# Kernel tuning notes

Hardware: AMD Instinct MI355X
Metric: run time of the kernel (lower is better)

The kernel has to match this reference:

```python
import jax, jax.numpy as jnp
import numpy as np
import math

GROUPS = 32  # min(256 // 4, 32)
EPS = 1e-5

def group_norm(x, w, b):
    B, C, H, W = x.shape
    xg = x.reshape(B, GROUPS, C // GROUPS, H, W)
    mean = jnp.mean(xg, axis=(2, 3, 4), keepdims=True)
    var = jnp.var(xg, axis=(2, 3, 4), keepdims=True)
    xn = ((xg - mean) * jax.lax.rsqrt(var + EPS)).reshape(B, C, H, W)
    return xn * w[None, :, None, None] + b[None, :, None, None]

def nin(x, W, b):
    # 1x1 projection: [B,C,H,W] x [C,D] -> [B,D,H,W]
    return jnp.einsum('bchw,cd->bdhw', x, W) + b[None, :, None, None]

def setup_inputs() -> dict:
    key = jax.random.key(0)
    ks = jax.random.split(key, 5)
    C = 256
    scale = 1.0 / math.sqrt(C)
    return {
        'x': jax.random.normal(ks[0], (4, C, 64, 64), dtype=jnp.float32),
        'gn_w': jnp.ones((C,), jnp.float32),
        'gn_b': jnp.zeros((C,), jnp.float32),
        'Wq': jax.random.normal(ks[1], (C, C), jnp.float32) * scale,
        'bq': jnp.zeros((C,), jnp.float32),
        'Wk': jax.random.normal(ks[2], (C, C), jnp.float32) * scale,
        'bk': jnp.zeros((C,), jnp.float32),
        'Wv': jax.random.normal(ks[3], (C, C), jnp.float32) * scale,
        'bv': jnp.zeros((C,), jnp.float32),
        'Wp': jax.random.normal(ks[4], (C, C), jnp.float32) * scale,
        'bp': jnp.zeros((C,), jnp.float32),
    }

def reference(x, gn_w, gn_b, Wq, bq, Wk, bk, Wv, bv, Wp, bp):
    B, C, H, W = x.shape
    h = group_norm(x, gn_w, gn_b)
    q = nin(h, Wq, bq).reshape(B, C, H * W)
    k = nin(h, Wk, bk).reshape(B, C, H * W)
    v = nin(h, Wv, bv).reshape(B, C, H * W)
    # attention logits: [B, HW, HW]
    w = jnp.einsum('bcn,bcm->bnm', q, k) * (C ** -0.5)
    w = jax.nn.softmax(w, axis=-1)
    h_out = jnp.einsum('bnm,bcm->bcn', w, v).reshape(B, C, H, W)
    h_out = nin(h_out, Wp, bp)
    out = x + h_out
    return out / math.sqrt(2.0)  # skip_rescale=True
```

## Files before the change

kernel.cpp:

```cpp
#include <hip/hip_runtime.h>
#include <math.h>


#define BB 4
#define CCH 256
#define NSP 4096
#define EPSV 1e-5f
#define ATTN_SCALE 0.0625f
#define RSQRT2 0.70710678118654752440f
#define KSPLIT 2
#define TILES_PER_PART 32

typedef __attribute__((ext_vector_type(8))) short bf16x8;
typedef __attribute__((ext_vector_type(4))) float f32x4;

typedef __attribute__((address_space(1))) void gvoid;
typedef __attribute__((address_space(3))) void lvoid;
__device__ __forceinline__ void dma16(const void* g, void* l) {
  __builtin_amdgcn_global_load_lds((gvoid*)g, (lvoid*)l, 16, 0, 0);
}

__device__ __forceinline__ short f2bf(float f) {
  union { float f; unsigned u; } a; a.f = f;
  unsigned r = a.u + 0x7fffu + ((a.u >> 16) & 1u);
  return (short)(r >> 16);
}
__device__ __forceinline__ float bf2f(short s) {
  union { unsigned u; float f; } a;
  a.u = ((unsigned)(unsigned short)s) << 16;
  return a.f;
}
__device__ __forceinline__ unsigned cvt_pk_bf16(float lo, float hi) {
  unsigned r;
  asm("v_cvt_pk_bf16_f32 %0, %1, %2" : "=v"(r) : "v"(lo), "v"(hi));
  return r;
}

__global__ __launch_bounds__(256) void gn_stats(
    const float* __restrict__ x, float* __restrict__ stats) {
  int b = blockIdx.x >> 5;
  int g = blockIdx.x & 31;
  size_t base = ((size_t)b * CCH + (size_t)g * 8) * NSP;
  const float4* xv = (const float4*)(x + base);
  int tid = threadIdx.x;
  float s = 0.f, ss = 0.f;
  for (int i = tid; i < 8192; i += 256) {
    float4 v = xv[i];
    s += (v.x + v.y) + (v.z + v.w);
    ss += (v.x * v.x + v.y * v.y) + (v.z * v.z + v.w * v.w);
  }
#pragma unroll
  for (int off = 32; off > 0; off >>= 1) {
    s += __shfl_down(s, off, 64);
    ss += __shfl_down(ss, off, 64);
  }
  __shared__ float rs[4], rss[4];
  int wv = tid >> 6;
  if ((tid & 63) == 0) { rs[wv] = s; rss[wv] = ss; }
  __syncthreads();
  if (tid == 0) {
    float S = rs[0] + rs[1] + rs[2] + rs[3];
    float SS = rss[0] + rss[1] + rss[2] + rss[3];
    float mean = S * (1.f / 32768.f);
    float var = SS * (1.f / 32768.f) - mean * mean;
    stats[(b * 32 + g) * 2 + 0] = mean;
    stats[(b * 32 + g) * 2 + 1] = rsqrtf(var + EPSV);
  }
}

__global__ __launch_bounds__(256) void prep_w(
    const float* __restrict__ Wq, const float* __restrict__ Wk,
    const float* __restrict__ Wv, const float* __restrict__ Wp,
    short* __restrict__ wts) {
  __shared__ float T[64][65];
  int c0 = blockIdx.x * 64, d0 = blockIdx.y * 64;
  int wz = blockIdx.z;
  const float* W = (wz == 0) ? Wq : (wz == 1) ? Wk : (wz == 2) ? Wv : Wp;
  short* wt = wts + (size_t)wz * CCH * CCH;
  int tid = threadIdx.x;
#pragma unroll
  for (int i = 0; i < 16; ++i) {
    int idx = tid + 256 * i;
    int row = idx >> 6, col = idx & 63;
    T[row][col] = W[(size_t)(c0 + row) * CCH + d0 + col];
  }
  __syncthreads();
#pragma unroll
  for (int i = 0; i < 16; ++i) {
    int idx = tid + 256 * i;
    int dr = idx >> 6, cc = idx & 63;
    wt[(size_t)(d0 + dr) * CCH + c0 + cc] = f2bf(T[cc][dr]);
  }
}

__global__ __launch_bounds__(512) void qkvg_kernel(
    const float* __restrict__ x, const float* __restrict__ stats,
    const float* __restrict__ gw, const float* __restrict__ gb,
    const short* __restrict__ wqt, const short* __restrict__ wkt,
    const short* __restrict__ wvt,
    const float* __restrict__ bq, const float* __restrict__ bk,
    const float* __restrict__ bv,
    short* __restrict__ qo, short* __restrict__ ko, short* __restrict__ vo) {
  __shared__ __align__(16) unsigned char smem[52224];
  float (*Ts)[68] = (float(*)[68])smem;
  float* aco = (float*)(smem + 17408);
  float* bco = aco + 256;
  short* Hs = (short*)(smem + 19456);
  short* Fo = (short*)smem;

  int bx = blockIdx.x;
  int b = bx & 3, n0 = (bx >> 2) * 64;
  int tid = threadIdx.x;
  if (tid < 256) {
    int g = tid >> 3;
    float mean = stats[(b * 32 + g) * 2 + 0];
    float rstd = stats[(b * 32 + g) * 2 + 1];
    float a = gw[tid] * rstd;
    aco[tid] = a;
    bco[tid] = gb[tid] - mean * a;
  }
  __syncthreads();
  const float* xb = x + (size_t)b * CCH * NSP;
  for (int p = 0; p < 4; ++p) {
    int c0 = p * 64;
#pragma unroll
    for (int i = 0; i < 2; ++i) {
      int crow = (tid >> 4) + i * 32;
      int c = c0 + crow;
      float4 v = *(const float4*)&xb[(size_t)c * NSP + n0 + (tid & 15) * 4];
      float a = aco[c], bb = bco[c];
      v.x = v.x * a + bb; v.y = v.y * a + bb;
      v.z = v.z * a + bb; v.w = v.w * a + bb;
      *(float4*)&Ts[crow][(tid & 15) * 4] = v;
    }
    __syncthreads();
    {
      int n = tid >> 3, seg = tid & 7;
      int cb = seg * 8;
      bf16x8 r;
#pragma unroll
      for (int j = 0; j < 8; ++j) r[j] = f2bf(Ts[cb + j][n]);
      int chunk = (c0 + cb) >> 3;
      *(bf16x8*)(Hs + n * 256 + ((chunk ^ (n & 7)) * 8)) = r;
    }
    __syncthreads();
  }
  int w = tid >> 6, lane = tid & 63, quad = lane >> 4, l16 = lane & 15;
  int wr = w & 3, h = w >> 2;
  bf16x8 a_h[8];
  {
    int row = wr * 16 + l16;
#pragma unroll
    for (int kc = 0; kc < 8; ++kc)
      a_h[kc] = *(bf16x8*)(Hs + row * 256 + (((kc * 4 + quad) ^ (row & 7)) * 8));
  }
  __syncthreads();
  for (int op = 0; op < 3; ++op) {
    const short* wt = (op == 0) ? wqt : (op == 1) ? wkt : wvt;
    const float* bias = (op == 0) ? bq : (op == 1) ? bk : bv;
    f32x4 acc[8];
#pragma unroll
    for (int mb = 0; mb < 8; ++mb) acc[mb] = (f32x4){0.f, 0.f, 0.f, 0.f};
#pragma unroll 4
    for (int mb = 0; mb < 8; ++mb) {
      const short* wp = wt + (size_t)((h * 8 + mb) * 16 + l16) * CCH + quad * 8;
#pragma unroll
      for (int kc = 0; kc < 8; ++kc) {
        bf16x8 af = *(const bf16x8*)(wp + kc * 32);
        acc[mb] = __builtin_amdgcn_mfma_f32_16x16x32_bf16(af, a_h[kc], acc[mb], 0, 0, 0);
      }
    }
    int n = n0 + wr * 16 + l16;
    if (op == 2) {
      short* ob = vo + (size_t)b * CCH * NSP;
      int mm = n & 63, m0_ = n & ~63;
      int mb_ = mm >> 4, qq = (mm >> 2) & 3, rr2 = mm & 3;
      int lc = (mb_ & 1) * 4 + qq;
      int jj = (mb_ >> 1) * 4 + rr2;
      int basen = m0_ + jj;
#pragma unroll
      for (int mb = 0; mb < 8; ++mb)
#pragma unroll
        for (int r = 0; r < 4; ++r) {
          int d = (h * 8 + mb) * 16 + quad * 4 + r;
          ob[(size_t)d * NSP + basen + ((lc ^ (d & 7)) << 3)] =
              f2bf(acc[mb][r] + bias[d]);
        }
    } else {
      float sc = (op == 0) ? ATTN_SCALE : 1.f;
      int nl = wr * 16 + l16;
#pragma unroll
      for (int mb = 0; mb < 8; ++mb)
#pragma unroll
        for (int r = 0; r < 4; ++r) {
          int d = (h * 8 + mb) * 16 + quad * 4 + r;
          Fo[nl * 264 + d] = f2bf((acc[mb][r] + bias[d]) * sc);
        }
      __syncthreads();
      short* ob = ((op == 0) ? qo : ko) + (size_t)b * NSP * CCH;
      {
        int row = tid >> 3, seg = tid & 7, r7 = row & 7;
        short* dst = ob + (size_t)(n0 + row) * CCH + seg * 32;
#pragma unroll
        for (int i = 0; i < 4; ++i) {
          int xch = seg * 4 + i;
          int cs = (xch & 24) | ((xch & 7) ^ r7);
          *(bf16x8*)(dst + i * 8) = *(bf16x8*)(Fo + row * 264 + cs * 8);
        }
      }
      __syncthreads();
    }
  }
}

__global__ __launch_bounds__(512, 1) void attn_kernel(
    const short* __restrict__ q, const short* __restrict__ k,
    const short* __restrict__ v, short* __restrict__ po,
    float* __restrict__ pm, float* __restrict__ pl) {
  __shared__ __align__(16) unsigned char smem[131072];
  short* Ks0 = (short*)smem;
  short* Ks1 = (short*)(smem + 32768);
  short* Vs0 = (short*)(smem + 65536);
  short* Vs1 = (short*)(smem + 98304);
  short* Fo  = (short*)smem;

  int bx = blockIdx.x;
  int grp = bx & 7;
  int b = grp & 3;
  int kh = grp >> 2;
  int n0 = ((bx >> 3) & 31) << 7;
  const short* qb = q + (size_t)b * NSP * CCH;
  const short* kb = k + (size_t)b * NSP * CCH;
  const char*  vbB = (const char*)(v + (size_t)b * CCH * NSP);
  int tid = threadIdx.x;
  int w = tid >> 6, lane = tid & 63, quad = lane >> 4, l16 = lane & 15;
  int mbase = kh * TILES_PER_PART * 64;

  bf16x8 a_q[8];
#pragma unroll
  for (int p = 0; p < 2; ++p) {
#pragma unroll
    for (int i = 0; i < 4; ++i) {
      int off = tid * 16 + i * 8192;
      dma16((const char*)(qb + (size_t)(n0 + p * 64) * CCH) + off,
            (char*)Ks0 + off);
    }
    __syncthreads();
    if ((w >> 2) == p) {
      int row = (w & 3) * 16 + l16;
#pragma unroll
      for (int kc = 0; kc < 8; ++kc)
        a_q[kc] = *(bf16x8*)(Ks0 + row * 256 + (((kc * 4 + quad) ^ (row & 7)) * 8));
    }
    __syncthreads();
  }

#pragma unroll
  for (int i = 0; i < 4; ++i) {
    int off = tid * 16 + i * 8192;
    dma16((const char*)(kb + (size_t)mbase * CCH) + off, (char*)Ks0 + off);
    int c = off >> 7, inrow = off & 127;
    dma16(vbB + (size_t)c * (NSP * 2) + (size_t)mbase * 2 + inrow,
          (char*)Vs0 + off);
  }
  __syncthreads();
#pragma unroll
  for (int i = 0; i < 4; ++i) {
    int off = tid * 16 + i * 8192;
    dma16((const char*)(kb + (size_t)(mbase + 64) * CCH) + off,
          (char*)Ks1 + off);
  }
  f32x4 s_prev[4];
#pragma unroll
  for (int mb = 0; mb < 4; ++mb) s_prev[mb] = (f32x4){0.f, 0.f, 0.f, 0.f};
  __builtin_amdgcn_s_setprio(1);
#pragma unroll
  for (int kc = 0; kc < 8; ++kc) {
#pragma unroll
    for (int mb = 0; mb < 4; ++mb) {
      int row = mb * 16 + l16;
      bf16x8 kf = *(bf16x8*)(Ks0 + row * 256 + (((kc * 4 + quad) ^ (row & 7)) * 8));
      s_prev[mb] = __builtin_amdgcn_mfma_f32_16x16x32_bf16(kf, a_q[kc], s_prev[mb], 0, 0, 0);
    }
  }
  __builtin_amdgcn_s_setprio(0);
  float mx_c = -1e30f;
#pragma unroll
  for (int mb = 0; mb < 4; ++mb)
#pragma unroll
    for (int r = 0; r < 4; ++r) mx_c = fmaxf(mx_c, s_prev[mb][r]);
  mx_c = fmaxf(mx_c, __shfl_xor(mx_c, 16));
  mx_c = fmaxf(mx_c, __shfl_xor(mx_c, 32));

  f32x4 accO[16];
#pragma unroll
  for (int cb = 0; cb < 16; ++cb) accO[cb] = (f32x4){0.f, 0.f, 0.f, 0.f};
  float m_run = -1e30f, l_run = 0.f;
  int pc0 = quad ^ (l16 & 7);
  int pc1 = (4 + quad) ^ (l16 & 7);

#pragma unroll 1
  for (int t = 0; t < TILES_PER_PART; ++t) {
    __syncthreads();
    short* Kd = (t & 1) ? Ks1 : Ks0;
    short* Kr = (t & 1) ? Ks0 : Ks1;
    short* Vd = (t & 1) ? Vs0 : Vs1;
    short* Vr = (t & 1) ? Vs1 : Vs0;
    if (t + 2 < TILES_PER_PART) {
      const char* kp = (const char*)(kb + (size_t)(mbase + (t + 2) * 64) * CCH);
#pragma unroll
      for (int i = 0; i < 4; ++i) {
        int off = tid * 16 + i * 8192;
        dma16(kp + off, (char*)Kd + off);
      }
    }
    if (t + 1 < TILES_PER_PART) {
      int m0 = mbase + (t + 1) * 64;
#pragma unroll
      for (int i = 0; i < 4; ++i) {
        int off = tid * 16 + i * 8192;
        int c = off >> 7, inrow = off & 127;
        dma16(vbB + (size_t)c * (NSP * 2) + (size_t)m0 * 2 + inrow,
              (char*)Vd + off);
      }
    }
    f32x4 sn[4];
#pragma unroll
    for (int mb = 0; mb < 4; ++mb) sn[mb] = (f32x4){0.f, 0.f, 0.f, 0.f};
    if (t + 1 < TILES_PER_PART) {
      __builtin_amdgcn_s_setprio(1);
#pragma unroll
      for (int kc = 0; kc < 8; ++kc) {
#pragma unroll
        for (int mb = 0; mb < 4; ++mb) {
          int row = mb * 16 + l16;
          bf16x8 kf = *(bf16x8*)(Kr + row * 256 + (((kc * 4 + quad) ^ (row & 7)) * 8));
          sn[mb] = __builtin_amdgcn_mfma_f32_16x16x32_bf16(kf, a_q[kc], sn[mb], 0, 0, 0);
        }
      }
      __builtin_amdgcn_s_setprio(0);
    }
    if (!__all(mx_c - m_run <= 8.f)) {
      float mnew = fmaxf(m_run, mx_c);
      float alpha = __expf(m_run - mnew);
#pragma unroll
      for (int cb = 0; cb < 16; ++cb) accO[cb] *= alpha;
      l_run *= alpha;
      m_run = mnew;
    }
    float ls = 0.f;
#pragma unroll
    for (int mb = 0; mb < 4; ++mb)
#pragma unroll
      for (int r = 0; r < 4; ++r) {
        float p = __expf(s_prev[mb][r] - m_run);
        ls += p;
        s_prev[mb][r] = p;
      }
    ls += __shfl_xor(ls, 16);
    ls += __shfl_xor(ls, 32);
    l_run += ls;
    union { unsigned u[4]; bf16x8 v; } pw0, pw1;
    pw0.u[0] = cvt_pk_bf16(s_prev[0][0], s_prev[0][1]);
    pw0.u[1] = cvt_pk_bf16(s_prev[0][2], s_prev[0][3]);
    pw0.u[2] = cvt_pk_bf16(s_prev[2][0], s_prev[2][1]);
    pw0.u[3] = cvt_pk_bf16(s_prev[2][2], s_prev[2][3]);
    pw1.u[0] = cvt_pk_bf16(s_prev[1][0], s_prev[1][1]);
    pw1.u[1] = cvt_pk_bf16(s_prev[1][2], s_prev[1][3]);
    pw1.u[2] = cvt_pk_bf16(s_prev[3][0], s_prev[3][1]);
    pw1.u[3] = cvt_pk_bf16(s_prev[3][2], s_prev[3][3]);
    __builtin_amdgcn_s_setprio(1);
#pragma unroll
    for (int cb = 0; cb < 16; ++cb) {
      bf16x8 vf = *(bf16x8*)(Vr + (cb * 16 + l16) * 64 + pc0 * 8);
      accO[cb] = __builtin_amdgcn_mfma_f32_16x16x32_bf16(vf, pw0.v, accO[cb], 0, 0, 0);
    }
#pragma unroll
    for (int cb = 0; cb < 16; ++cb) {
      bf16x8 vf = *(bf16x8*)(Vr + (cb * 16 + l16) * 64 + pc1 * 8);
      accO[cb] = __builtin_amdgcn_mfma_f32_16x16x32_bf16(vf, pw1.v, accO[cb], 0, 0, 0);
    }
    __builtin_amdgcn_s_setprio(0);
    if (t + 1 < TILES_PER_PART) {
      float mxn = -1e30f;
#pragma unroll
      for (int mb = 0; mb < 4; ++mb)
#pragma unroll
        for (int r = 0; r < 4; ++r) mxn = fmaxf(mxn, sn[mb][r]);
      mxn = fmaxf(mxn, __shfl_xor(mxn, 16));
      mxn = fmaxf(mxn, __shfl_xor(mxn, 32));
      mx_c = mxn;
    }
#pragma unroll
    for (int mb = 0; mb < 4; ++mb) s_prev[mb] = sn[mb];
  }
  size_t sbase = ((size_t)kh * BB + b) * NSP + n0;
  if (quad == 0) {
    pm[sbase + w * 16 + l16] = m_run;
    pl[sbase + w * 16 + l16] = l_run;
  }
  float linv = 1.f / l_run;
  short* ob = po + ((size_t)kh * BB + b) * NSP * CCH;
#pragma unroll
  for (int p = 0; p < 2; ++p) {
    __syncthreads();
    if ((w >> 2) == p) {
      int nloc = (w & 3) * 16 + l16;
#pragma unroll
      for (int cb = 0; cb < 16; ++cb)
#pragma unroll
        for (int r = 0; r < 4; ++r)
          Fo[nloc * 264 + cb * 16 + quad * 4 + r] = f2bf(accO[cb][r] * linv);
    }
    __syncthreads();
    int row = tid >> 3, seg = tid & 7;
    short* dst = ob + (size_t)(n0 + p * 64 + row) * CCH + seg * 32;
#pragma unroll
    for (int i = 0; i < 4; ++i)
      *(bf16x8*)(dst + i * 8) = *(bf16x8*)(Fo + row * 264 + seg * 32 + i * 8);
  }
}

__global__ __launch_bounds__(256) void proj_kernel(
    const short* __restrict__ po, const float* __restrict__ pm,
    const float* __restrict__ pl, const short* __restrict__ wpt,
    const float* __restrict__ bp, const float* __restrict__ x,
    float* __restrict__ out) {
  int n0 = blockIdx.x * 64;
  int dh = blockIdx.y * 128;
  int b = blockIdx.z;
  int tid = threadIdx.x;
  int w = tid >> 6, lane = tid & 63, quad = lane >> 4, l16 = lane & 15;
  int n = n0 + w * 16 + l16;

  float wgt[KSPLIT];
  {
    float m[KSPLIT];
    float M = -1e30f;
#pragma unroll
    for (int s = 0; s < KSPLIT; ++s) {
      m[s] = pm[((size_t)s * BB + b) * NSP + n];
      M = fmaxf(M, m[s]);
    }
    float wsum = 0.f;
#pragma unroll
    for (int s = 0; s < KSPLIT; ++s) {
      wgt[s] = __expf(m[s] - M) * pl[((size_t)s * BB + b) * NSP + n];
      wsum += wgt[s];
    }
    float linv = 1.f / wsum;
#pragma unroll
    for (int s = 0; s < KSPLIT; ++s) wgt[s] *= linv;
  }

  f32x4 acc[8];
#pragma unroll
  for (int mb = 0; mb < 8; ++mb) acc[mb] = (f32x4){0.f, 0.f, 0.f, 0.f};

  const short* pob = po + ((size_t)b * NSP + n) * CCH;
#pragma unroll 2
  for (int kc = 0; kc < 8; ++kc) {
    int coff = kc * 32 + quad * 8;
    float e[8];
#pragma unroll
    for (int i = 0; i < 8; ++i) e[i] = 0.f;
#pragma unroll
    for (int s = 0; s < KSPLIT; ++s) {
      bf16x8 f = *(const bf16x8*)(pob + (size_t)s * BB * NSP * CCH + coff);
#pragma unroll
      for (int i = 0; i < 8; ++i) e[i] += wgt[s] * bf2f(f[i]);
    }
    bf16x8 bm;
#pragma unroll
    for (int i = 0; i < 8; ++i) bm[i] = f2bf(e[i]);
#pragma unroll
    for (int mb = 0; mb < 8; ++mb) {
      bf16x8 af = *(const bf16x8*)(wpt + (size_t)(dh + mb * 16 + l16) * CCH + coff);
      acc[mb] = __builtin_amdgcn_mfma_f32_16x16x32_bf16(af, bm, acc[mb], 0, 0, 0);
    }
  }
#pragma unroll
  for (int mb = 0; mb < 8; ++mb) {
#pragma unroll
    for (int r = 0; r < 4; ++r) {
      int d = dh + mb * 16 + quad * 4 + r;
      size_t off = ((size_t)b * CCH + d) * NSP + n;
      out[off] = (acc[mb][r] + bp[d] + x[off]) * RSQRT2;
    }
  }
}

extern "C" void kernel_launch(void* const* d_in, const int* in_sizes, int n_in,
                              void* d_out, int out_size, void* d_ws, size_t ws_size,
                              hipStream_t stream) {
  const float* x  = (const float*)d_in[0];
  const float* gw = (const float*)d_in[1];
  const float* gb = (const float*)d_in[2];
  const float* Wq = (const float*)d_in[3];
  const float* bq = (const float*)d_in[4];
  const float* Wk = (const float*)d_in[5];
  const float* bk = (const float*)d_in[6];
  const float* Wv = (const float*)d_in[7];
  const float* bv = (const float*)d_in[8];
  const float* Wp = (const float*)d_in[9];
  const float* bp = (const float*)d_in[10];
  float* out = (float*)d_out;

  const size_t SZ = (size_t)BB * CCH * NSP;
  short* qb  = (short*)d_ws;
  short* kb  = qb + SZ;
  short* vb  = kb + SZ;
  short* poT = vb + SZ;
  float* pm  = (float*)(poT + (size_t)KSPLIT * SZ);
  float* pl  = pm + (size_t)KSPLIT * BB * NSP;
  float* stats = pl + (size_t)KSPLIT * BB * NSP;
  short* wts = (short*)(stats + BB * 64);
  short* wqt = wts;
  short* wkt = wts + (size_t)CCH * CCH;
  short* wvt = wts + (size_t)2 * CCH * CCH;
  short* wpt = wts + (size_t)3 * CCH * CCH;

  gn_stats<<<dim3(BB * 32), dim3(256), 0, stream>>>(x, stats);
  prep_w<<<dim3(4, 4, 4), dim3(256), 0, stream>>>(Wq, Wk, Wv, Wp, wts);
  qkvg_kernel<<<dim3(256), dim3(512), 0, stream>>>(
      x, stats, gw, gb, wqt, wkt, wvt, bq, bk, bv, qb, kb, vb);
  attn_kernel<<<dim3(BB * 32 * KSPLIT), dim3(512), 0, stream>>>(
      qb, kb, vb, poT, pm, pl);
  proj_kernel<<<dim3(64, 2, BB), dim3(256), 0, stream>>>(
      poT, pm, pl, wpt, bp, x, out);
}
```

Measured before the change: 275.4 us.

## Halve attention block to 4 waves, each wave handling 32 query rows

The attention kernel now launches 256 threads instead of 512, and each wave computes two 16-row query subtiles. Every K and V fragment read from LDS feeds two MFMAs, which halves LDS read traffic per unit of compute. The DMA loops and the output writeback are adjusted to the smaller thread count. The cost is roughly double the accumulator and score registers per wave, with fewer waves per CU available to hide latency.

```diff
diff --git a/kernel.cpp b/kernel.cpp
--- a/kernel.cpp
+++ b/kernel.cpp
@@ -213,7 +213,7 @@
   }
 }
 
-__global__ __launch_bounds__(512, 1) void attn_kernel(
+__global__ __launch_bounds__(256, 1) void attn_kernel(
     const short* __restrict__ q, const short* __restrict__ k,
     const short* __restrict__ v, short* __restrict__ po,
     float* __restrict__ pm, float* __restrict__ pl) {
@@ -236,28 +236,32 @@
   int w = tid >> 6, lane = tid & 63, quad = lane >> 4, l16 = lane & 15;
   int mbase = kh * TILES_PER_PART * 64;
 
-  bf16x8 a_q[8];
+  bf16x8 a_q[2][8];
 #pragma unroll
   for (int p = 0; p < 2; ++p) {
 #pragma unroll
-    for (int i = 0; i < 4; ++i) {
-      int off = tid * 16 + i * 8192;
+    for (int i = 0; i < 8; ++i) {
+      int off = tid * 16 + i * 4096;
       dma16((const char*)(qb + (size_t)(n0 + p * 64) * CCH) + off,
             (char*)Ks0 + off);
     }
     __syncthreads();
-    if ((w >> 2) == p) {
-      int row = (w & 3) * 16 + l16;
-#pragma unroll
-      for (int kc = 0; kc < 8; ++kc)
-        a_q[kc] = *(bf16x8*)(Ks0 + row * 256 + (((kc * 4 + quad) ^ (row & 7)) * 8));
-    }
-    __syncthreads();
-  }
-
-#pragma unroll
-  for (int i = 0; i < 4; ++i) {
-    int off = tid * 16 + i * 8192;
+    if ((w >> 1) == p) {
+#pragma unroll
+      for (int qh = 0; qh < 2; ++qh) {
+        int row = (w & 1) * 32 + qh * 16 + l16;
+#pragma unroll
+        for (int kc = 0; kc < 8; ++kc)
+          a_q[qh][kc] =
+              *(bf16x8*)(Ks0 + row * 256 + (((kc * 4 + quad) ^ (row & 7)) * 8));
+      }
+    }
+    __syncthreads();
+  }
+
+#pragma unroll
+  for (int i = 0; i < 8; ++i) {
+    int off = tid * 16 + i * 4096;
     dma16((const char*)(kb + (size_t)mbase * CCH) + off, (char*)Ks0 + off);
     int c = off >> 7, inrow = off & 127;
     dma16(vbB + (size_t)c * (NSP * 2) + (size_t)mbase * 2 + inrow,
@@ -265,14 +269,16 @@
   }
   __syncthreads();
 #pragma unroll
-  for (int i = 0; i < 4; ++i) {
-    int off = tid * 16 + i * 8192;
+  for (int i = 0; i < 8; ++i) {
+    int off = tid * 16 + i * 4096;
     dma16((const char*)(kb + (size_t)(mbase + 64) * CCH) + off,
           (char*)Ks1 + off);
   }
-  f32x4 s_prev[4];
-#pragma unroll
-  for (int mb = 0; mb < 4; ++mb) s_prev[mb] = (f32x4){0.f, 0.f, 0.f, 0.f};
+  f32x4 s_prev[4][2];
+#pragma unroll
+  for (int mb = 0; mb < 4; ++mb)
+#pragma unroll
+    for (int qh = 0; qh < 2; ++qh) s_prev[mb][qh] = (f32x4){0.f, 0.f, 0.f, 0.f};
   __builtin_amdgcn_s_setprio(1);
 #pragma unroll
   for (int kc = 0; kc < 8; ++kc) {
@@ -280,22 +286,32 @@
     for (int mb = 0; mb < 4; ++mb) {
       int row = mb * 16 + l16;
       bf16x8 kf = *(bf16x8*)(Ks0 + row * 256 + (((kc * 4 + quad) ^ (row & 7)) * 8));
-      s_prev[mb] = __builtin_amdgcn_mfma_f32_16x16x32_bf16(kf, a_q[kc], s_prev[mb], 0, 0, 0);
+#pragma unroll
+      for (int qh = 0; qh < 2; ++qh)
+        s_prev[mb][qh] = __builtin_amdgcn_mfma_f32_16x16x32_bf16(
+            kf, a_q[qh][kc], s_prev[mb][qh], 0, 0, 0);
     }
   }
   __builtin_amdgcn_s_setprio(0);
-  float mx_c = -1e30f;
-#pragma unroll
-  for (int mb = 0; mb < 4; ++mb)
-#pragma unroll
-    for (int r = 0; r < 4; ++r) mx_c = fmaxf(mx_c, s_prev[mb][r]);
-  mx_c = fmaxf(mx_c, __shfl_xor(mx_c, 16));
-  mx_c = fmaxf(mx_c, __shfl_xor(mx_c, 32));
-
-  f32x4 accO[16];
-#pragma unroll
-  for (int cb = 0; cb < 16; ++cb) accO[cb] = (f32x4){0.f, 0.f, 0.f, 0.f};
-  float m_run = -1e30f, l_run = 0.f;
+  float mx_c[2];
+#pragma unroll
+  for (int qh = 0; qh < 2; ++qh) {
+    float mx = -1e30f;
+#pragma unroll
+    for (int mb = 0; mb < 4; ++mb)
+#pragma unroll
+      for (int r = 0; r < 4; ++r) mx = fmaxf(mx, s_prev[mb][qh][r]);
+    mx = fmaxf(mx, __shfl_xor(mx, 16));
+    mx = fmaxf(mx, __shfl_xor(mx, 32));
+    mx_c[qh] = mx;
+  }
+
+  f32x4 accO[16][2];
+#pragma unroll
+  for (int cb = 0; cb < 16; ++cb)
+#pragma unroll
+    for (int qh = 0; qh < 2; ++qh) accO[cb][qh] = (f32x4){0.f, 0.f, 0.f, 0.f};
+  float m_run[2] = {-1e30f, -1e30f}, l_run[2] = {0.f, 0.f};
   int pc0 = quad ^ (l16 & 7);
   int pc1 = (4 + quad) ^ (l16 & 7);
 
@@ -309,24 +325,26 @@
     if (t + 2 < TILES_PER_PART) {
       const char* kp = (const char*)(kb + (size_t)(mbase + (t + 2) * 64) * CCH);
 #pragma unroll
-      for (int i = 0; i < 4; ++i) {
-        int off = tid * 16 + i * 8192;
+      for (int i = 0; i < 8; ++i) {
+        int off = tid * 16 + i * 4096;
         dma16(kp + off, (char*)Kd + off);
       }
     }
     if (t + 1 < TILES_PER_PART) {
       int m0 = mbase + (t + 1) * 64;
 #pragma unroll
-      for (int i = 0; i < 4; ++i) {
-        int off = tid * 16 + i * 8192;
+      for (int i = 0; i < 8; ++i) {
+        int off = tid * 16 + i * 4096;
         int c = off >> 7, inrow = off & 127;
         dma16(vbB + (size_t)c * (NSP * 2) + (size_t)m0 * 2 + inrow,
               (char*)Vd + off);
       }
     }
-    f32x4 sn[4];
-#pragma unroll
-    for (int mb = 0; mb < 4; ++mb) sn[mb] = (f32x4){0.f, 0.f, 0.f, 0.f};
+    f32x4 sn[4][2];
+#pragma unroll
+    for (int mb = 0; mb < 4; ++mb)
+#pragma unroll
+      for (int qh = 0; qh < 2; ++qh) sn[mb][qh] = (f32x4){0.f, 0.f, 0.f, 0.f};
     if (t + 1 < TILES_PER_PART) {
       __builtin_amdgcn_s_setprio(1);
 #pragma unroll
@@ -335,89 +353,120 @@
         for (int mb = 0; mb < 4; ++mb) {
           int row = mb * 16 + l16;
           bf16x8 kf = *(bf16x8*)(Kr + row * 256 + (((kc * 4 + quad) ^ (row & 7)) * 8));
-          sn[mb] = __builtin_amdgcn_mfma_f32_16x16x32_bf16(kf, a_q[kc], sn[mb], 0, 0, 0);
+#pragma unroll
+          for (int qh = 0; qh < 2; ++qh)
+            sn[mb][qh] = __builtin_amdgcn_mfma_f32_16x16x32_bf16(
+                kf, a_q[qh][kc], sn[mb][qh], 0, 0, 0);
         }
       }
       __builtin_amdgcn_s_setprio(0);
     }
-    if (!__all(mx_c - m_run <= 8.f)) {
-      float mnew = fmaxf(m_run, mx_c);
-      float alpha = __expf(m_run - mnew);
-#pragma unroll
-      for (int cb = 0; cb < 16; ++cb) accO[cb] *= alpha;
-      l_run *= alpha;
-      m_run = mnew;
-    }
-    float ls = 0.f;
-#pragma unroll
-    for (int mb = 0; mb < 4; ++mb)
-#pragma unroll
-      for (int r = 0; r < 4; ++r) {
-        float p = __expf(s_prev[mb][r] - m_run);
-        ls += p;
-        s_prev[mb][r] = p;
-      }
-    ls += __shfl_xor(ls, 16);
-    ls += __shfl_xor(ls, 32);
-    l_run += ls;
-    union { unsigned u[4]; bf16x8 v; } pw0, pw1;
-    pw0.u[0] = cvt_pk_bf16(s_prev[0][0], s_prev[0][1]);
-    pw0.u[1] = cvt_pk_bf16(s_prev[0][2], s_prev[0][3]);
-    pw0.u[2] = cvt_pk_bf16(s_prev[2][0], s_prev[2][1]);
-    pw0.u[3] = cvt_pk_bf16(s_prev[2][2], s_prev[2][3]);
-    pw1.u[0] = cvt_pk_bf16(s_prev[1][0], s_prev[1][1]);
-    pw1.u[1] = cvt_pk_bf16(s_prev[1][2], s_prev[1][3]);
-    pw1.u[2] = cvt_pk_bf16(s_prev[3][0], s_prev[3][1]);
-    pw1.u[3] = cvt_pk_bf16(s_prev[3][2], s_prev[3][3]);
+    bool grow = (mx_c[0] - m_run[0] > 8.f) || (mx_c[1] - m_run[1] > 8.f);
+    if (__any(grow)) {
+#pragma unroll
+      for (int qh = 0; qh < 2; ++qh) {
+        float mnew = fmaxf(m_run[qh], mx_c[qh]);
+        float alpha = __expf(m_run[qh] - mnew);
+#pragma unroll
+        for (int cb = 0; cb < 16; ++cb) accO[cb][qh] *= alpha;
+        l_run[qh] *= alpha;
+        m_run[qh] = mnew;
+      }
+    }
+#pragma unroll
+    for (int qh = 0; qh < 2; ++qh) {
+      float ls = 0.f;
+#pragma unroll
+      for (int mb = 0; mb < 4; ++mb)
+#pragma unroll
+        for (int r = 0; r < 4; ++r) {
+          float p = __expf(s_prev[mb][qh][r] - m_run[qh]);
+          ls += p;
+          s_prev[mb][qh][r] = p;
+        }
+      ls += __shfl_xor(ls, 16);
+      ls += __shfl_xor(ls, 32);
+      l_run[qh] += ls;
+    }
+    union { unsigned u[4]; bf16x8 v; } pw0[2], pw1[2];
+#pragma unroll
+    for (int qh = 0; qh < 2; ++qh) {
+      pw0[qh].u[0] = cvt_pk_bf16(s_prev[0][qh][0], s_prev[0][qh][1]);
+      pw0[qh].u[1] = cvt_pk_bf16(s_prev[0][qh][2], s_prev[0][qh][3]);
+      pw0[qh].u[2] = cvt_pk_bf16(s_prev[2][qh][0], s_prev[2][qh][1]);
+      pw0[qh].u[3] = cvt_pk_bf16(s_prev[2][qh][2], s_prev[2][qh][3]);
+      pw1[qh].u[0] = cvt_pk_bf16(s_prev[1][qh][0], s_prev[1][qh][1]);
+      pw1[qh].u[1] = cvt_pk_bf16(s_prev[1][qh][2], s_prev[1][qh][3]);
+      pw1[qh].u[2] = cvt_pk_bf16(s_prev[3][qh][0], s_prev[3][qh][1]);
+      pw1[qh].u[3] = cvt_pk_bf16(s_prev[3][qh][2], s_prev[3][qh][3]);
+    }
     __builtin_amdgcn_s_setprio(1);
 #pragma unroll
     for (int cb = 0; cb < 16; ++cb) {
       bf16x8 vf = *(bf16x8*)(Vr + (cb * 16 + l16) * 64 + pc0 * 8);
-      accO[cb] = __builtin_amdgcn_mfma_f32_16x16x32_bf16(vf, pw0.v, accO[cb], 0, 0, 0);
+#pragma unroll
+      for (int qh = 0; qh < 2; ++qh)
+        accO[cb][qh] = __builtin_amdgcn_mfma_f32_16x16x32_bf16(
+            vf, pw0[qh].v, accO[cb][qh], 0, 0, 0);
     }
 #pragma unroll
     for (int cb = 0; cb < 16; ++cb) {
       bf16x8 vf = *(bf16x8*)(Vr + (cb * 16 + l16) * 64 + pc1 * 8);
-      accO[cb] = __builtin_amdgcn_mfma_f32_16x16x32_bf16(vf, pw1.v, accO[cb], 0, 0, 0);
+#pragma unroll
+      for (int qh = 0; qh < 2; ++qh)
+        accO[cb][qh] = __builtin_amdgcn_mfma_f32_16x16x32_bf16(
+            vf, pw1[qh].v, accO[cb][qh], 0, 0, 0);
     }
     __builtin_amdgcn_s_setprio(0);
     if (t + 1 < TILES_PER_PART) {
-      float mxn = -1e30f;
-#pragma unroll
-      for (int mb = 0; mb < 4; ++mb)
-#pragma unroll
-        for (int r = 0; r < 4; ++r) mxn = fmaxf(mxn, sn[mb][r]);
-      mxn = fmaxf(mxn, __shfl_xor(mxn, 16));
-      mxn = fmaxf(mxn, __shfl_xor(mxn, 32));
-      mx_c = mxn;
-    }
-#pragma unroll
-    for (int mb = 0; mb < 4; ++mb) s_prev[mb] = sn[mb];
+#pragma unroll
+      for (int qh = 0; qh < 2; ++qh) {
+        float mxn = -1e30f;
+#pragma unroll
+        for (int mb = 0; mb < 4; ++mb)
+#pragma unroll
+          for (int r = 0; r < 4; ++r) mxn = fmaxf(mxn, sn[mb][qh][r]);
+        mxn = fmaxf(mxn, __shfl_xor(mxn, 16));
+        mxn = fmaxf(mxn, __shfl_xor(mxn, 32));
+        mx_c[qh] = mxn;
+      }
+    }
+#pragma unroll
+    for (int mb = 0; mb < 4; ++mb)
+#pragma unroll
+      for (int qh = 0; qh < 2; ++qh) s_prev[mb][qh] = sn[mb][qh];
   }
   size_t sbase = ((size_t)kh * BB + b) * NSP + n0;
   if (quad == 0) {
-    pm[sbase + w * 16 + l16] = m_run;
-    pl[sbase + w * 16 + l16] = l_run;
-  }
-  float linv = 1.f / l_run;
+#pragma unroll
+    for (int qh = 0; qh < 2; ++qh) {
+      pm[sbase + w * 32 + qh * 16 + l16] = m_run[qh];
+      pl[sbase + w * 32 + qh * 16 + l16] = l_run[qh];
+    }
+  }
   short* ob = po + ((size_t)kh * BB + b) * NSP * CCH;
 #pragma unroll
   for (int p = 0; p < 2; ++p) {
     __syncthreads();
-    if ((w >> 2) == p) {
-      int nloc = (w & 3) * 16 + l16;
-#pragma unroll
-      for (int cb = 0; cb < 16; ++cb)
-#pragma unroll
-        for (int r = 0; r < 4; ++r)
-          Fo[nloc * 264 + cb * 16 + quad * 4 + r] = f2bf(accO[cb][r] * linv);
-    }
-    __syncthreads();
-    int row = tid >> 3, seg = tid & 7;
-    short* dst = ob + (size_t)(n0 + p * 64 + row) * CCH + seg * 32;
-#pragma unroll
-    for (int i = 0; i < 4; ++i)
-      *(bf16x8*)(dst + i * 8) = *(bf16x8*)(Fo + row * 264 + seg * 32 + i * 8);
+    if ((w >> 1) == p) {
+#pragma unroll
+      for (int qh = 0; qh < 2; ++qh) {
+        int nloc = (w & 1) * 32 + qh * 16 + l16;
+        float linv = 1.f / l_run[qh];
+#pragma unroll
+        for (int cb = 0; cb < 16; ++cb)
+#pragma unroll
+          for (int r = 0; r < 4; ++r)
+            Fo[nloc * 264 + cb * 16 + quad * 4 + r] =
+                f2bf(accO[cb][qh][r] * linv);
+      }
+    }
+    __syncthreads();
+    int row = tid >> 2, seg = tid & 3;
+    short* dst = ob + (size_t)(n0 + p * 64 + row) * CCH + seg * 64;
+#pragma unroll
+    for (int i = 0; i < 8; ++i)
+      *(bf16x8*)(dst + i * 8) = *(bf16x8*)(Fo + row * 264 + seg * 64 + i * 8);
   }
 }
 
@@ -524,7 +573,7 @@
   prep_w<<<dim3(4, 4, 4), dim3(256), 0, stream>>>(Wq, Wk, Wv, Wp, wts);
   qkvg_kernel<<<dim3(256), dim3(512), 0, stream>>>(
       x, stats, gw, gb, wqt, wkt, wvt, bq, bk, bv, qb, kb, vb);
-  attn_kernel<<<dim3(BB * 32 * KSPLIT), dim3(512), 0, stream>>>(
+  attn_kernel<<<dim3(BB * 32 * KSPLIT), dim3(256), 0, stream>>>(
       qb, kb, vb, poT, pm, pl);
   proj_kernel<<<dim3(64, 2, BB), dim3(256), 0, stream>>>(
       poT, pm, pl, wpt, bp, x, out);
```

After: 307.6 us. +11.7%, slower.

## Merge GN stats and weight prep kernels, split stats, remap attention blocks

Applied to the files above, without the earlier changes.

Fuses the group-norm statistics and weight transpose/convert kernels into one launch. Statistics are now split into two half-groups per block (256 blocks instead of 128), with the final mean/rstd computed in the QKV kernel from the partial sums. The attention grid mapping changes so that the key-split index is the slowest dimension, and the running max is recomputed from the current scores instead of being carried over from the previous iteration. This removes one launch and improves parallelism in the stats pass, but may move the max computation onto the critical path inside the attention loop.

```diff
diff --git a/kernel.cpp b/kernel.cpp
--- a/kernel.cpp
+++ b/kernel.cpp
@@ -36,60 +36,57 @@
   return r;
 }
 
-__global__ __launch_bounds__(256) void gn_stats(
-    const float* __restrict__ x, float* __restrict__ stats) {
-  int b = blockIdx.x >> 5;
-  int g = blockIdx.x & 31;
-  size_t base = ((size_t)b * CCH + (size_t)g * 8) * NSP;
-  const float4* xv = (const float4*)(x + base);
-  int tid = threadIdx.x;
-  float s = 0.f, ss = 0.f;
-  for (int i = tid; i < 8192; i += 256) {
-    float4 v = xv[i];
-    s += (v.x + v.y) + (v.z + v.w);
-    ss += (v.x * v.x + v.y * v.y) + (v.z * v.z + v.w * v.w);
-  }
-#pragma unroll
-  for (int off = 32; off > 0; off >>= 1) {
-    s += __shfl_down(s, off, 64);
-    ss += __shfl_down(ss, off, 64);
-  }
-  __shared__ float rs[4], rss[4];
-  int wv = tid >> 6;
-  if ((tid & 63) == 0) { rs[wv] = s; rss[wv] = ss; }
-  __syncthreads();
-  if (tid == 0) {
-    float S = rs[0] + rs[1] + rs[2] + rs[3];
-    float SS = rss[0] + rss[1] + rss[2] + rss[3];
-    float mean = S * (1.f / 32768.f);
-    float var = SS * (1.f / 32768.f) - mean * mean;
-    stats[(b * 32 + g) * 2 + 0] = mean;
-    stats[(b * 32 + g) * 2 + 1] = rsqrtf(var + EPSV);
-  }
-}
-
-__global__ __launch_bounds__(256) void prep_w(
+__global__ __launch_bounds__(256) void prep_all(
+    const float* __restrict__ x,
     const float* __restrict__ Wq, const float* __restrict__ Wk,
     const float* __restrict__ Wv, const float* __restrict__ Wp,
-    short* __restrict__ wts) {
+    float* __restrict__ stats, short* __restrict__ wts) {
   __shared__ float T[64][65];
-  int c0 = blockIdx.x * 64, d0 = blockIdx.y * 64;
-  int wz = blockIdx.z;
-  const float* W = (wz == 0) ? Wq : (wz == 1) ? Wk : (wz == 2) ? Wv : Wp;
-  short* wt = wts + (size_t)wz * CCH * CCH;
+  int bid = blockIdx.x;
   int tid = threadIdx.x;
-#pragma unroll
-  for (int i = 0; i < 16; ++i) {
-    int idx = tid + 256 * i;
-    int row = idx >> 6, col = idx & 63;
-    T[row][col] = W[(size_t)(c0 + row) * CCH + d0 + col];
-  }
-  __syncthreads();
-#pragma unroll
-  for (int i = 0; i < 16; ++i) {
-    int idx = tid + 256 * i;
-    int dr = idx >> 6, cc = idx & 63;
-    wt[(size_t)(d0 + dr) * CCH + c0 + cc] = f2bf(T[cc][dr]);
+  if (bid < 256) {
+    int b = bid >> 6, g = (bid >> 1) & 31, h = bid & 1;
+    size_t base = ((size_t)b * CCH + (size_t)g * 8 + (size_t)h * 4) * NSP;
+    const float4* xv = (const float4*)(x + base);
+    float s = 0.f, ss = 0.f;
+    for (int i = tid; i < 4096; i += 256) {
+      float4 v = xv[i];
+      s += (v.x + v.y) + (v.z + v.w);
+      ss += (v.x * v.x + v.y * v.y) + (v.z * v.z + v.w * v.w);
+    }
+#pragma unroll
+    for (int off = 32; off > 0; off >>= 1) {
+      s += __shfl_down(s, off, 64);
+      ss += __shfl_down(ss, off, 64);
+    }
+    int wv = tid >> 6;
+    if ((tid & 63) == 0) { T[0][wv] = s; T[0][4 + wv] = ss; }
+    __syncthreads();
+    if (tid == 0) {
+      float S = T[0][0] + T[0][1] + T[0][2] + T[0][3];
+      float SS = T[0][4] + T[0][5] + T[0][6] + T[0][7];
+      stats[((b * 32 + g) * 2 + h) * 2 + 0] = S;
+      stats[((b * 32 + g) * 2 + h) * 2 + 1] = SS;
+    }
+  } else {
+    int wid = bid - 256;
+    int c0 = (wid & 3) * 64, d0 = ((wid >> 2) & 3) * 64;
+    int wz = wid >> 4;
+    const float* W = (wz == 0) ? Wq : (wz == 1) ? Wk : (wz == 2) ? Wv : Wp;
+    short* wt = wts + (size_t)wz * CCH * CCH;
+#pragma unroll
+    for (int i = 0; i < 16; ++i) {
+      int idx = tid + 256 * i;
+      int row = idx >> 6, col = idx & 63;
+      T[row][col] = W[(size_t)(c0 + row) * CCH + d0 + col];
+    }
+    __syncthreads();
+#pragma unroll
+    for (int i = 0; i < 16; ++i) {
+      int idx = tid + 256 * i;
+      int dr = idx >> 6, cc = idx & 63;
+      wt[(size_t)(d0 + dr) * CCH + c0 + cc] = f2bf(T[cc][dr]);
+    }
   }
 }
 
@@ -113,8 +110,11 @@
   int tid = threadIdx.x;
   if (tid < 256) {
     int g = tid >> 3;
-    float mean = stats[(b * 32 + g) * 2 + 0];
-    float rstd = stats[(b * 32 + g) * 2 + 1];
+    const float* sp = stats + (size_t)(b * 32 + g) * 4;
+    float S = sp[0] + sp[2], SS = sp[1] + sp[3];
+    float mean = S * (1.f / 32768.f);
+    float var = SS * (1.f / 32768.f) - mean * mean;
+    float rstd = rsqrtf(var + EPSV);
     float a = gw[tid] * rstd;
     aco[tid] = a;
     bco[tid] = gb[tid] - mean * a;
@@ -225,10 +225,9 @@
   short* Fo  = (short*)smem;
 
   int bx = blockIdx.x;
-  int grp = bx & 7;
-  int b = grp & 3;
-  int kh = grp >> 2;
-  int n0 = ((bx >> 3) & 31) << 7;
+  int b = bx & 3;
+  int n0 = ((bx >> 2) & 31) << 7;
+  int kh = bx >> 7;
   const short* qb = q + (size_t)b * NSP * CCH;
   const short* kb = k + (size_t)b * NSP * CCH;
   const char*  vbB = (const char*)(v + (size_t)b * CCH * NSP);
@@ -284,13 +283,6 @@
     }
   }
   __builtin_amdgcn_s_setprio(0);
-  float mx_c = -1e30f;
-#pragma unroll
-  for (int mb = 0; mb < 4; ++mb)
-#pragma unroll
-    for (int r = 0; r < 4; ++r) mx_c = fmaxf(mx_c, s_prev[mb][r]);
-  mx_c = fmaxf(mx_c, __shfl_xor(mx_c, 16));
-  mx_c = fmaxf(mx_c, __shfl_xor(mx_c, 32));
 
   f32x4 accO[16];
 #pragma unroll
@@ -340,8 +332,15 @@
       }
       __builtin_amdgcn_s_setprio(0);
     }
-    if (!__all(mx_c - m_run <= 8.f)) {
-      float mnew = fmaxf(m_run, mx_c);
+    float mx = -1e30f;
+#pragma unroll
+    for (int mb = 0; mb < 4; ++mb)
+#pragma unroll
+      for (int r = 0; r < 4; ++r) mx = fmaxf(mx, s_prev[mb][r]);
+    mx = fmaxf(mx, __shfl_xor(mx, 16));
+    mx = fmaxf(mx, __shfl_xor(mx, 32));
+    if (!__all(mx - m_run <= 8.f)) {
+      float mnew = fmaxf(m_run, mx);
       float alpha = __expf(m_run - mnew);
 #pragma unroll
       for (int cb = 0; cb < 16; ++cb) accO[cb] *= alpha;
@@ -381,16 +380,6 @@
       accO[cb] = __builtin_amdgcn_mfma_f32_16x16x32_bf16(vf, pw1.v, accO[cb], 0, 0, 0);
     }
     __builtin_amdgcn_s_setprio(0);
-    if (t + 1 < TILES_PER_PART) {
-      float mxn = -1e30f;
-#pragma unroll
-      for (int mb = 0; mb < 4; ++mb)
-#pragma unroll
-        for (int r = 0; r < 4; ++r) mxn = fmaxf(mxn, sn[mb][r]);
-      mxn = fmaxf(mxn, __shfl_xor(mxn, 16));
-      mxn = fmaxf(mxn, __shfl_xor(mxn, 32));
-      mx_c = mxn;
-    }
 #pragma unroll
     for (int mb = 0; mb < 4; ++mb) s_prev[mb] = sn[mb];
   }
@@ -514,14 +503,13 @@
   float* pm  = (float*)(poT + (size_t)KSPLIT * SZ);
   float* pl  = pm + (size_t)KSPLIT * BB * NSP;
   float* stats = pl + (size_t)KSPLIT * BB * NSP;
-  short* wts = (short*)(stats + BB * 64);
+  short* wts = (short*)(stats + BB * 128);
   short* wqt = wts;
   short* wkt = wts + (size_t)CCH * CCH;
   short* wvt = wts + (size_t)2 * CCH * CCH;
   short* wpt = wts + (size_t)3 * CCH * CCH;
 
-  gn_stats<<<dim3(BB * 32), dim3(256), 0, stream>>>(x, stats);
-  prep_w<<<dim3(4, 4, 4), dim3(256), 0, stream>>>(Wq, Wk, Wv, Wp, wts);
+  prep_all<<<dim3(320), dim3(256), 0, stream>>>(x, Wq, Wk, Wv, Wp, stats, wts);
   qkvg_kernel<<<dim3(256), dim3(512), 0, stream>>>(
       x, stats, gw, gb, wqt, wkt, wvt, bq, bk, bv, qb, kb, vb);
   attn_kernel<<<dim3(BB * 32 * KSPLIT), dim3(512), 0, stream>>>(
```

Result: faster. 267.5 us (-2.9%).
